# Kernel optimization log

Hardware: AMD Instinct MI355X
Metric: run time of the kernel (lower is better)

## Reference

```python
import jax, jax.numpy as jnp
import numpy as np
from jax import lax

N_EMBD = 4096
N_EXPERTS = 64


def setup_inputs() -> dict:
    key = jax.random.key(0)
    kx, kw = jax.random.split(key)
    x = jax.random.normal(kx, (4, 4096, N_EMBD), dtype=jnp.float32)
    # nn.Linear(n_embd, n_experts, bias=False) -> weight shape [n_experts, n_embd]
    W = jax.random.normal(kw, (N_EXPERTS, N_EMBD), dtype=jnp.float32) * (1.0 / np.sqrt(N_EMBD))
    return {"x": x, "W": W}


def reference(x, W):
    # logits = x @ W^T : [B, S, n_experts]
    logits = jnp.einsum('bsd,ed->bse', x, W)
    topk_vals, topk_idx = lax.top_k(logits, 2)  # [B, S, 2]
    gates = jax.nn.softmax(topk_vals, axis=-1)  # softmax over just the top-2 values
    return (topk_idx, gates)
```

## Files before the change

### kernel.cpp

```cpp
#include <hip/hip_runtime.h>
#include <math.h>

#define N_EMBD    4096
#define N_EXPERTS 64
#define N_TOKENS  16384
#define TAU       1e-3f
#define NT_BLK    32
#define KS        4
#define K_BLK     (N_EMBD / KS)
#define BK2       64
#define NT2       (K_BLK / BK2)

typedef __attribute__((ext_vector_type(8))) short bf16x8;
typedef __attribute__((ext_vector_type(4))) float f32x4;

#define MFMA16 __builtin_amdgcn_mfma_f32_16x16x32_bf16

struct hl_pair { unsigned h, l; };

__device__ __forceinline__ hl_pair split_pair(float f0, float f1) {
    unsigned u0 = __builtin_bit_cast(unsigned, f0);
    unsigned u1 = __builtin_bit_cast(unsigned, f1);
    unsigned r0 = u0 + 0x7FFFu + ((u0 >> 16) & 1u);
    unsigned r1 = u1 + 0x7FFFu + ((u1 >> 16) & 1u);
    hl_pair p;
    p.h = (r0 >> 16) | (r1 & 0xFFFF0000u);
    float h0 = __builtin_bit_cast(float, r0 & 0xFFFF0000u);
    float h1 = __builtin_bit_cast(float, r1 & 0xFFFF0000u);
    float l0 = f0 - h0;
    float l1 = f1 - h1;
    unsigned v0 = __builtin_bit_cast(unsigned, l0);
    unsigned v1 = __builtin_bit_cast(unsigned, l1);
    unsigned s0 = v0 + 0x7FFFu + ((v0 >> 16) & 1u);
    unsigned s1 = v1 + 0x7FFFu + ((v1 >> 16) & 1u);
    p.l = (s0 >> 16) | (s1 & 0xFFFF0000u);
    return p;
}

__global__ void w_pack_bf16(const float* __restrict__ W,
                            uint4* __restrict__ Bpack,
                            int* __restrict__ flags) {
    int tid = blockIdx.x * blockDim.x + threadIdx.x;
    if (tid == 0) flags[0] = 0;
    int lane = tid & 63;
    int nt   = (tid >> 6) & 3;
    int ks   = tid >> 8;
    int e = nt * 16 + (lane & 15);
    int k = ks * 32 + ((lane >> 4) << 3);
    const float* src = W + (size_t)e * N_EMBD + k;
    uint4 hp, lp;
    hl_pair p0 = split_pair(src[0], src[1]);
    hl_pair p1 = split_pair(src[2], src[3]);
    hl_pair p2 = split_pair(src[4], src[5]);
    hl_pair p3 = split_pair(src[6], src[7]);
    hp.x = p0.h; lp.x = p0.l;
    hp.y = p1.h; lp.y = p1.l;
    hp.z = p2.h; lp.z = p2.l;
    hp.w = p3.h; lp.w = p3.l;
    size_t F = (size_t)ks * 8 + nt * 2;
    Bpack[F * 64 + lane]       = hp;
    Bpack[(F + 1) * 64 + lane] = lp;
}

__device__ __forceinline__ void store_split8(char* buf, int off, f32x4 a, f32x4 b) {
    hl_pair p0 = split_pair(a.x, a.y);
    hl_pair p1 = split_pair(a.z, a.w);
    hl_pair p2 = split_pair(b.x, b.y);
    hl_pair p3 = split_pair(b.z, b.w);
    uint4 h, l;
    h.x = p0.h; h.y = p1.h; h.z = p2.h; h.w = p3.h;
    l.x = p0.l; l.y = p1.l; l.z = p2.l; l.w = p3.l;
    *(uint4*)(buf + off)        = h;
    *(uint4*)(buf + off + 4096) = l;
}

__global__ __launch_bounds__(256, 8) void router_gemm(
        const float* __restrict__ x,
        const uint4* __restrict__ Bpack,
        float* __restrict__ partial) {
    __shared__ __align__(16) char ldsA[2 * 8192];

    const int tid  = threadIdx.x;
    const int lane = tid & 63;
    const int w    = tid >> 6;
    const int kq   = blockIdx.x & 3;
    const int tok0 = (blockIdx.x >> 2) * NT_BLK;
    const int l15 = lane & 15, l16 = lane >> 4;

    const int row_w = tid >> 3;
    const int c8    = tid & 7;
    const f32x4* g = (const f32x4*)(x + (size_t)(tok0 + row_w) * N_EMBD
                                      + kq * K_BLK + c8 * 8);
    const int wo = row_w * 128 + ((c8 * 16) ^ ((row_w & 7) << 4));

    const int swz_r = (l15 & 7) << 4;
    const int ro0 = l15 * 128 + ((l16 * 16)      ^ swz_r);
    const int ro1 = l15 * 128 + ((64 + l16 * 16) ^ swz_r);

    f32x4 acc0 = {0.f, 0.f, 0.f, 0.f};
    f32x4 acc1 = {0.f, 0.f, 0.f, 0.f};
    f32x4 ra0, ra1;

    char* buf0 = ldsA;
    char* buf1 = ldsA + 8192;

    const uint4* bbase = Bpack + ((size_t)(kq * 32) * 8 + w * 2) * 64 + lane;

#define LOADA(t) { ra0 = g[(t) * 16]; ra1 = g[(t) * 16 + 1]; }
#define STOREA(buf) store_split8(buf, wo, ra0, ra1)
#define COMPUTE(bufR, tt) {                                                   \
    const uint4* bq = bbase + (size_t)(tt) * 1024;                            \
    uint4 bh0q = bq[0];   uint4 bl0q = bq[64];                                \
    uint4 bh1q = bq[512]; uint4 bl1q = bq[576];                               \
    bf16x8 bh0 = __builtin_bit_cast(bf16x8, bh0q);                            \
    bf16x8 bl0 = __builtin_bit_cast(bf16x8, bl0q);                            \
    bf16x8 bh1 = __builtin_bit_cast(bf16x8, bh1q);                            \
    bf16x8 bl1 = __builtin_bit_cast(bf16x8, bl1q);                            \
    bf16x8 a;                                                                 \
    a = *(const bf16x8*)((bufR) + ro0);                                       \
    acc0 = MFMA16(a, bh0, acc0, 0, 0, 0);                                     \
    acc0 = MFMA16(a, bl0, acc0, 0, 0, 0);                                     \
    a = *(const bf16x8*)((bufR) + ro0 + 4096);                                \
    acc0 = MFMA16(a, bh0, acc0, 0, 0, 0);                                     \
    a = *(const bf16x8*)((bufR) + ro0 + 2048);                                \
    acc1 = MFMA16(a, bh0, acc1, 0, 0, 0);                                     \
    acc1 = MFMA16(a, bl0, acc1, 0, 0, 0);                                     \
    a = *(const bf16x8*)((bufR) + ro0 + 2048 + 4096);                         \
    acc1 = MFMA16(a, bh0, acc1, 0, 0, 0);                                     \
    a = *(const bf16x8*)((bufR) + ro1);                                       \
    acc0 = MFMA16(a, bh1, acc0, 0, 0, 0);                                     \
    acc0 = MFMA16(a, bl1, acc0, 0, 0, 0);                                     \
    a = *(const bf16x8*)((bufR) + ro1 + 4096);                                \
    acc0 = MFMA16(a, bh1, acc0, 0, 0, 0);                                     \
    a = *(const bf16x8*)((bufR) + ro1 + 2048);                                \
    acc1 = MFMA16(a, bh1, acc1, 0, 0, 0);                                     \
    acc1 = MFMA16(a, bl1, acc1, 0, 0, 0);                                     \
    a = *(const bf16x8*)((bufR) + ro1 + 2048 + 4096);                         \
    acc1 = MFMA16(a, bh1, acc1, 0, 0, 0);                                     \
}

    LOADA(0);
    STOREA(buf0);
    LOADA(1);
    asm volatile("s_waitcnt lgkmcnt(0)" ::: "memory");
    __builtin_amdgcn_s_barrier();
    __builtin_amdgcn_sched_barrier(0);

    for (int t = 0; t < NT2; t += 2) {
        COMPUTE(buf0, t);
        STOREA(buf1);
        if (t + 2 < NT2) LOADA(t + 2);
        asm volatile("s_waitcnt lgkmcnt(0)" ::: "memory");
        __builtin_amdgcn_s_barrier();
        __builtin_amdgcn_sched_barrier(0);

        COMPUTE(buf1, t + 1);
        if (t + 2 < NT2) {
            STOREA(buf0);
            if (t + 3 < NT2) LOADA(t + 3);
            asm volatile("s_waitcnt lgkmcnt(0)" ::: "memory");
            __builtin_amdgcn_s_barrier();
            __builtin_amdgcn_sched_barrier(0);
        }
    }
#undef LOADA
#undef STOREA
#undef COMPUTE

    float* po = partial + ((size_t)kq * N_TOKENS + tok0) * 64 + w * 16 + l15;
#pragma unroll
    for (int j = 0; j < 4; ++j) {
        po[(size_t)(l16 * 4 + j) * 64]        = acc0[j];
        po[(size_t)(16 + l16 * 4 + j) * 64]   = acc1[j];
    }
}

__global__ void finalize(const float* __restrict__ partial,
                         float* __restrict__ out,
                         int* __restrict__ flags) {
    const int lane = threadIdx.x & 63;
    const int tok  = blockIdx.x * 4 + (threadIdx.x >> 6);

    float v = partial[(size_t)tok * 64 + lane]
            + partial[((size_t)N_TOKENS + tok) * 64 + lane]
            + partial[((size_t)2 * N_TOKENS + tok) * 64 + lane]
            + partial[((size_t)3 * N_TOKENS + tok) * 64 + lane];

    float m1 = v; int i1 = lane;
#pragma unroll
    for (int off = 32; off; off >>= 1) {
        float ov = __shfl_xor(m1, off); int oi = __shfl_xor(i1, off);
        if (ov > m1 || (ov == m1 && oi < i1)) { m1 = ov; i1 = oi; }
    }
    float m2 = (lane == i1) ? -INFINITY : v; int i2 = lane;
#pragma unroll
    for (int off = 32; off; off >>= 1) {
        float ov = __shfl_xor(m2, off); int oi = __shfl_xor(i2, off);
        if (ov > m2 || (ov == m2 && oi < i2)) { m2 = ov; i2 = oi; }
    }
    float m3 = (lane == i1 || lane == i2) ? -INFINITY : v;
#pragma unroll
    for (int off = 32; off; off >>= 1)
        m3 = fmaxf(m3, __shfl_xor(m3, off));

    if (lane == 0) {
        float e2  = __expf(m2 - m1);
        float inv = 1.0f / (1.0f + e2);
        float2 idx = make_float2((float)i1, (float)i2);
        float2 gts = make_float2(inv, e2 * inv);
        *(float2*)(out + 2 * tok) = idx;
        *(float2*)(out + 2 * N_TOKENS + 2 * tok) = gts;
        if ((m1 - m2 < TAU) || (m2 - m3 < TAU)) {
            int p = atomicAdd(flags, 1);
            if (p < N_TOKENS) flags[1 + p] = tok;
        }
    }
}

__global__ __launch_bounds__(256) void refine(const float* __restrict__ x,
                                              const float* __restrict__ W,
                                              const int* __restrict__ flags,
                                              float* __restrict__ out) {
    __shared__ double redd[64];
    const int lane = threadIdx.x & 63;
    const int wv   = threadIdx.x >> 6;
    int cnt = flags[0];
    if (cnt > N_TOKENS) cnt = N_TOKENS;

    for (int i = blockIdx.x; i < cnt; i += gridDim.x) {
        const int tok = flags[1 + i];
        const float4* xr4 = (const float4*)(x + (size_t)tok * N_EMBD);
#pragma unroll
        for (int ee = 0; ee < 16; ++ee) {
            const int e = wv * 16 + ee;
            const float4* wr = (const float4*)(W + (size_t)e * N_EMBD);
            double acc = 0.0;
#pragma unroll 4
            for (int c = 0; c < 16; ++c) {
                float4 xv = xr4[c * 64 + lane];
                float4 wq = wr[c * 64 + lane];
                acc += (double)xv.x * wq.x + (double)xv.y * wq.y
                     + (double)xv.z * wq.z + (double)xv.w * wq.w;
            }
#pragma unroll
            for (int off = 32; off; off >>= 1)
                acc += __shfl_xor(acc, off);
            if (lane == 0) redd[e] = acc;
        }
        __syncthreads();
        if (wv == 0) {
            double v = redd[lane];
            double m1 = v; int i1 = lane;
#pragma unroll
            for (int off = 32; off; off >>= 1) {
                double ov = __shfl_xor(m1, off); int oi = __shfl_xor(i1, off);
                if (ov > m1 || (ov == m1 && oi < i1)) { m1 = ov; i1 = oi; }
            }
            double m2 = (lane == i1) ? -INFINITY : v; int i2 = lane;
#pragma unroll
            for (int off = 32; off; off >>= 1) {
                double ov = __shfl_xor(m2, off); int oi = __shfl_xor(i2, off);
                if (ov > m2 || (ov == m2 && oi < i2)) { m2 = ov; i2 = oi; }
            }
            if (lane == 0) {
                double e2  = exp(m2 - m1);
                double inv = 1.0 / (1.0 + e2);
                out[2 * tok + 0] = (float)i1;
                out[2 * tok + 1] = (float)i2;
                out[2 * N_TOKENS + 2 * tok + 0] = (float)inv;
                out[2 * N_TOKENS + 2 * tok + 1] = (float)(e2 * inv);
            }
        }
        __syncthreads();
    }
}

extern "C" void kernel_launch(void* const* d_in, const int* in_sizes, int n_in,
                              void* d_out, int out_size, void* d_ws, size_t ws_size,
                              hipStream_t stream) {
    const float* x = (const float*)d_in[0];
    const float* W = (const float*)d_in[1];
    float* out = (float*)d_out;

    uint4* Bpack   = (uint4*)d_ws;
    int*   flags   = (int*)((char*)d_ws + (1u << 20));
    float* partial = (float*)((char*)d_ws + (2u << 20));

    w_pack_bf16<<<128, 256, 0, stream>>>(W, Bpack, flags);
    router_gemm<<<(N_TOKENS / NT_BLK) * KS, 256, 0, stream>>>(x, Bpack, partial);
    finalize   <<<N_TOKENS / 4, 256, 0, stream>>>(partial, out, flags);
    refine     <<<128, 256, 0, stream>>>(x, W, flags, out);
}
```

Baseline: 109.7 us.

## Halve K-split, widen K tile to 128, prefetch B fragments into registers

```diff
diff --git a/kernel.cpp b/kernel.cpp
--- a/kernel.cpp
+++ b/kernel.cpp
@@ -6,10 +6,12 @@
 #define N_TOKENS  16384
 #define TAU       1e-3f
 #define NT_BLK    32
-#define KS        4
+#define KS        2
 #define K_BLK     (N_EMBD / KS)
-#define BK2       64
-#define NT2       (K_BLK / BK2)
+#define BK        128
+#define NT2       (K_BLK / BK)
+#define PLANE     8192
+#define BUFB      (2 * PLANE)
 
 typedef __attribute__((ext_vector_type(8))) short bf16x8;
 typedef __attribute__((ext_vector_type(4))) float f32x4;
@@ -62,116 +64,123 @@
     Bpack[(F + 1) * 64 + lane] = lp;
 }
 
-__device__ __forceinline__ void store_split8(char* buf, int off, f32x4 a, f32x4 b) {
-    hl_pair p0 = split_pair(a.x, a.y);
-    hl_pair p1 = split_pair(a.z, a.w);
-    hl_pair p2 = split_pair(b.x, b.y);
-    hl_pair p3 = split_pair(b.z, b.w);
-    uint4 h, l;
-    h.x = p0.h; h.y = p1.h; h.z = p2.h; h.w = p3.h;
-    l.x = p0.l; l.y = p1.l; l.z = p2.l; l.w = p3.l;
-    *(uint4*)(buf + off)        = h;
-    *(uint4*)(buf + off + 4096) = l;
-}
-
-__global__ __launch_bounds__(256, 8) void router_gemm(
+__device__ __forceinline__ void store_chunk(char* buf, int off, f32x4 v) {
+    hl_pair p01 = split_pair(v.x, v.y);
+    hl_pair p23 = split_pair(v.z, v.w);
+    uint2 hw, lw;
+    hw.x = p01.h; hw.y = p23.h;
+    lw.x = p01.l; lw.y = p23.l;
+    *(uint2*)(buf + off)         = hw;
+    *(uint2*)(buf + off + PLANE) = lw;
+}
+
+__global__ __launch_bounds__(256, 4) void router_gemm(
         const float* __restrict__ x,
         const uint4* __restrict__ Bpack,
         float* __restrict__ partial) {
-    __shared__ __align__(16) char ldsA[2 * 8192];
+    __shared__ __align__(16) char ldsA[2 * BUFB];
 
     const int tid  = threadIdx.x;
     const int lane = tid & 63;
     const int w    = tid >> 6;
-    const int kq   = blockIdx.x & 3;
-    const int tok0 = (blockIdx.x >> 2) * NT_BLK;
+    const int kq   = blockIdx.x & 1;
+    const int tok0 = (blockIdx.x >> 1) * NT_BLK;
     const int l15 = lane & 15, l16 = lane >> 4;
 
     const int row_w = tid >> 3;
     const int c8    = tid & 7;
     const f32x4* g = (const f32x4*)(x + (size_t)(tok0 + row_w) * N_EMBD
-                                      + kq * K_BLK + c8 * 8);
-    const int wo = row_w * 128 + ((c8 * 16) ^ ((row_w & 7) << 4));
+                                      + kq * K_BLK) + c8;
+    const int swz = (row_w & 7) << 4;
+    int wo[4];
+#pragma unroll
+    for (int j = 0; j < 4; ++j)
+        wo[j] = row_w * 256 + (((c8 + 8 * j) * 8) ^ swz);
 
     const int swz_r = (l15 & 7) << 4;
-    const int ro0 = l15 * 128 + ((l16 * 16)      ^ swz_r);
-    const int ro1 = l15 * 128 + ((64 + l16 * 16) ^ swz_r);
+    int ro[4];
+#pragma unroll
+    for (int ksl = 0; ksl < 4; ++ksl)
+        ro[ksl] = l15 * 256 + ((l16 * 16 + ksl * 64) ^ swz_r);
 
     f32x4 acc0 = {0.f, 0.f, 0.f, 0.f};
     f32x4 acc1 = {0.f, 0.f, 0.f, 0.f};
-    f32x4 ra0, ra1;
+    f32x4 ra[4];
+    uint4 bah[4], bal[4], bbh[4], bbl[4];
 
     char* buf0 = ldsA;
-    char* buf1 = ldsA + 8192;
-
-    const uint4* bbase = Bpack + ((size_t)(kq * 32) * 8 + w * 2) * 64 + lane;
-
-#define LOADA(t) { ra0 = g[(t) * 16]; ra1 = g[(t) * 16 + 1]; }
-#define STOREA(buf) store_split8(buf, wo, ra0, ra1)
-#define COMPUTE(bufR, tt) {                                                   \
-    const uint4* bq = bbase + (size_t)(tt) * 1024;                            \
-    uint4 bh0q = bq[0];   uint4 bl0q = bq[64];                                \
-    uint4 bh1q = bq[512]; uint4 bl1q = bq[576];                               \
-    bf16x8 bh0 = __builtin_bit_cast(bf16x8, bh0q);                            \
-    bf16x8 bl0 = __builtin_bit_cast(bf16x8, bl0q);                            \
-    bf16x8 bh1 = __builtin_bit_cast(bf16x8, bh1q);                            \
-    bf16x8 bl1 = __builtin_bit_cast(bf16x8, bl1q);                            \
-    bf16x8 a;                                                                 \
-    a = *(const bf16x8*)((bufR) + ro0);                                       \
-    acc0 = MFMA16(a, bh0, acc0, 0, 0, 0);                                     \
-    acc0 = MFMA16(a, bl0, acc0, 0, 0, 0);                                     \
-    a = *(const bf16x8*)((bufR) + ro0 + 4096);                                \
-    acc0 = MFMA16(a, bh0, acc0, 0, 0, 0);                                     \
-    a = *(const bf16x8*)((bufR) + ro0 + 2048);                                \
-    acc1 = MFMA16(a, bh0, acc1, 0, 0, 0);                                     \
-    acc1 = MFMA16(a, bl0, acc1, 0, 0, 0);                                     \
-    a = *(const bf16x8*)((bufR) + ro0 + 2048 + 4096);                         \
-    acc1 = MFMA16(a, bh0, acc1, 0, 0, 0);                                     \
-    a = *(const bf16x8*)((bufR) + ro1);                                       \
-    acc0 = MFMA16(a, bh1, acc0, 0, 0, 0);                                     \
-    acc0 = MFMA16(a, bl1, acc0, 0, 0, 0);                                     \
-    a = *(const bf16x8*)((bufR) + ro1 + 4096);                                \
-    acc0 = MFMA16(a, bh1, acc0, 0, 0, 0);                                     \
-    a = *(const bf16x8*)((bufR) + ro1 + 2048);                                \
-    acc1 = MFMA16(a, bh1, acc1, 0, 0, 0);                                     \
-    acc1 = MFMA16(a, bl1, acc1, 0, 0, 0);                                     \
-    a = *(const bf16x8*)((bufR) + ro1 + 2048 + 4096);                         \
-    acc1 = MFMA16(a, bh1, acc1, 0, 0, 0);                                     \
-}
+    char* buf1 = ldsA + BUFB;
+
+#define LOADA(t) { _Pragma("unroll")                                          \
+    for (int j = 0; j < 4; ++j) ra[j] = g[(t) * 32 + j * 8]; }
+#define STOREA(buf) { _Pragma("unroll")                                       \
+    for (int j = 0; j < 4; ++j) store_chunk(buf, wo[j], ra[j]); }
+#define LOADB(H, L, tt) { const uint4* _q = Bpack                             \
+        + ((size_t)(kq * (K_BLK / 32) + (tt) * 4) * 8 + w * 2) * 64 + lane;   \
+    _Pragma("unroll")                                                         \
+    for (int ksl = 0; ksl < 4; ++ksl) {                                       \
+        H[ksl] = _q[ksl * 512]; L[ksl] = _q[ksl * 512 + 64]; } }
+#define COMPUTE(bufR, H, L) { _Pragma("unroll")                               \
+    for (int ksl = 0; ksl < 4; ++ksl) {                                       \
+        bf16x8 bh = __builtin_bit_cast(bf16x8, H[ksl]);                       \
+        bf16x8 bl = __builtin_bit_cast(bf16x8, L[ksl]);                       \
+        bf16x8 a;                                                             \
+        a = *(const bf16x8*)((bufR) + ro[ksl]);                               \
+        acc0 = MFMA16(a, bh, acc0, 0, 0, 0);                                  \
+        acc0 = MFMA16(a, bl, acc0, 0, 0, 0);                                  \
+        a = *(const bf16x8*)((bufR) + ro[ksl] + PLANE);                       \
+        acc0 = MFMA16(a, bh, acc0, 0, 0, 0);                                  \
+        a = *(const bf16x8*)((bufR) + ro[ksl] + 4096);                        \
+        acc1 = MFMA16(a, bh, acc1, 0, 0, 0);                                  \
+        acc1 = MFMA16(a, bl, acc1, 0, 0, 0);                                  \
+        a = *(const bf16x8*)((bufR) + ro[ksl] + 4096 + PLANE);                \
+        acc1 = MFMA16(a, bh, acc1, 0, 0, 0);                                  \
+    } }
 
     LOADA(0);
     STOREA(buf0);
+    LOADB(bah, bal, 0);
     LOADA(1);
+    __builtin_amdgcn_sched_barrier(0);
     asm volatile("s_waitcnt lgkmcnt(0)" ::: "memory");
     __builtin_amdgcn_s_barrier();
     __builtin_amdgcn_sched_barrier(0);
 
     for (int t = 0; t < NT2; t += 2) {
-        COMPUTE(buf0, t);
+        LOADB(bbh, bbl, t + 1);
+        __builtin_amdgcn_sched_barrier(0);
         STOREA(buf1);
         if (t + 2 < NT2) LOADA(t + 2);
+        __builtin_amdgcn_sched_barrier(0);
+        COMPUTE(buf0, bah, bal);
         asm volatile("s_waitcnt lgkmcnt(0)" ::: "memory");
         __builtin_amdgcn_s_barrier();
         __builtin_amdgcn_sched_barrier(0);
 
-        COMPUTE(buf1, t + 1);
         if (t + 2 < NT2) {
+            LOADB(bah, bal, t + 2);
+            __builtin_amdgcn_sched_barrier(0);
             STOREA(buf0);
             if (t + 3 < NT2) LOADA(t + 3);
+            __builtin_amdgcn_sched_barrier(0);
+            COMPUTE(buf1, bbh, bbl);
             asm volatile("s_waitcnt lgkmcnt(0)" ::: "memory");
             __builtin_amdgcn_s_barrier();
             __builtin_amdgcn_sched_barrier(0);
+        } else {
+            COMPUTE(buf1, bbh, bbl);
         }
     }
 #undef LOADA
 #undef STOREA
+#undef LOADB
 #undef COMPUTE
 
     float* po = partial + ((size_t)kq * N_TOKENS + tok0) * 64 + w * 16 + l15;
 #pragma unroll
     for (int j = 0; j < 4; ++j) {
-        po[(size_t)(l16 * 4 + j) * 64]        = acc0[j];
-        po[(size_t)(16 + l16 * 4 + j) * 64]   = acc1[j];
+        po[(size_t)(l16 * 4 + j) * 64]      = acc0[j];
+        po[(size_t)(16 + l16 * 4 + j) * 64] = acc1[j];
     }
 }
 
@@ -182,9 +191,7 @@
     const int tok  = blockIdx.x * 4 + (threadIdx.x >> 6);
 
     float v = partial[(size_t)tok * 64 + lane]
-            + partial[((size_t)N_TOKENS + tok) * 64 + lane]
-            + partial[((size_t)2 * N_TOKENS + tok) * 64 + lane]
-            + partial[((size_t)3 * N_TOKENS + tok) * 64 + lane];
+            + partial[((size_t)N_TOKENS + tok) * 64 + lane];
 
     float m1 = v; int i1 = lane;
 #pragma unroll
```

Measured after the change: 109.7 us. Within noise of the previous version (+0.0%).
